# Kernel tuning notes

Measured on AMD Instinct MI355X. Metric: run time of the kernel, lower is better.

Reference implementation:

```python
import jax, jax.numpy as jnp
import numpy as np

T, D_IN, D_OUT, R, S = 8192, 4096, 4096, 16, 16  # tokens, in, out, lora rank, n_stacks
GATE_THRESHOLD = 0.12


def setup_inputs() -> dict:
    key = jax.random.key(0)
    ks = jax.random.split(key, 6)
    x = jax.random.normal(ks[0], (T, D_IN), jnp.float32)
    W = jax.random.normal(ks[1], (D_OUT, D_IN), jnp.float32) * 0.02  # frozen linear weight
    b = jax.random.normal(ks[2], (D_OUT,), jnp.float32) * 0.02       # frozen linear bias
    A = jax.random.normal(ks[3], (S, R, D_IN), jnp.float32) * 0.02   # per-stack lora_A
    B = jax.random.normal(ks[4], (S, D_OUT, R), jnp.float32) * 0.02  # per-stack lora_B
    domain_weights = jax.random.uniform(ks[5], (S,), jnp.float32)    # sigmoid-router weights per domain
    stack_domain = jnp.arange(S, dtype=jnp.int32)                    # stack -> domain index (count=1 each)
    return {"x": x, "W": W, "b": b, "A": A, "B": B,
            "domain_weights": domain_weights, "stack_domain": stack_domain}


def reference(x, W, b, A, B, domain_weights, stack_domain):
    # base frozen linear: out = x @ W^T + b
    base = x @ W.T + b  # [T, D_OUT]
    # threshold-gated per-stack weights: w if w > GATE_THRESHOLD else 0
    g = jnp.where(domain_weights > GATE_THRESHOLD, domain_weights, 0.0)[stack_domain]  # [S]
    # grouped LoRA: stack(x) = (x @ A_s^T) @ B_s^T, combined with gate weights
    h = jnp.einsum('td,srd->str', x, A)          # [S, T, R]
    lora = jnp.einsum('s,str,sor->to', g, h, B)  # [T, D_OUT]
    # original wraps stack contributions in torch.no_grad()
    return base + jax.lax.stop_gradient(lora)
```

## Files before the change

### kernel.cpp

```cpp
#include <hip/hip_runtime.h>
#include <hip/hip_bf16.h>

typedef __bf16 bf16;
typedef __attribute__((ext_vector_type(8))) __bf16 bf16x8;
typedef __attribute__((ext_vector_type(4))) float f32x4;

#define T_TOK 8192
#define DIN   4096
#define DOUT  4096
#define RNK   16
#define NS    16
#define KLORA (NS * RNK)
#define GATE  0.12f

typedef __attribute__((address_space(1))) const void gconst_t;
typedef __attribute__((address_space(3))) void lds_t;

__device__ __forceinline__ void gload_lds16(const void* g, void* l) {
  __builtin_amdgcn_global_load_lds((gconst_t*)g, (lds_t*)l, 16, 0, 0);
}

#define BAR() do { asm volatile("" ::: "memory"); \
                   __builtin_amdgcn_s_barrier();  \
                   asm volatile("" ::: "memory"); } while (0)
#define VMW(n) asm volatile("s_waitcnt vmcnt(" #n ")" ::: "memory")


__global__ __launch_bounds__(256)
void cast_x_kernel(const float* __restrict__ x, bf16* __restrict__ xb) {
  const long i = ((long)blockIdx.x * 256 + threadIdx.x) * 8;
  const float4 v0 = *(const float4*)(x + i);
  const float4 v1 = *(const float4*)(x + i + 4);
  bf16x8 o;
  o[0] = (bf16)v0.x; o[1] = (bf16)v0.y; o[2] = (bf16)v0.z; o[3] = (bf16)v0.w;
  o[4] = (bf16)v1.x; o[5] = (bf16)v1.y; o[6] = (bf16)v1.z; o[7] = (bf16)v1.w;
  *(bf16x8*)(xb + i) = o;
}

__global__ __launch_bounds__(256)
void build_bg_kernel(const float* __restrict__ B, const float* __restrict__ dw,
                     const int* __restrict__ sd, bf16* __restrict__ bg) {
  const int t = blockIdx.x * 256 + threadIdx.x;
  const int o = t >> 8, k = t & 255, s = k >> 4, r = k & 15;
  const float w = dw[sd[s]];
  const float g = (w > GATE) ? w : 0.f;
  bg[t] = (bf16)(g * B[((size_t)s * DOUT + o) * RNK + r]);
}

__global__ __launch_bounds__(256)
void transpose_a_kernel(const float* __restrict__ A, bf16* __restrict__ at) {
  __shared__ float t[32][33];
  const int d0 = blockIdx.x * 32, k0 = blockIdx.y * 32;
  const int tx = threadIdx.x & 31, ty = threadIdx.x >> 5;
#pragma unroll
  for (int i = 0; i < 32; i += 8)
    t[ty + i][tx] = A[(size_t)(k0 + ty + i) * DIN + d0 + tx];
  __syncthreads();
#pragma unroll
  for (int i = 0; i < 32; i += 8)
    at[(size_t)(d0 + ty + i) * KLORA + k0 + tx] = (bf16)t[tx][ty + i];
}

__global__ __launch_bounds__(256)
void gemm_bt(const bf16* __restrict__ Am, const bf16* __restrict__ Bm,
             const float* __restrict__ extra, bf16* __restrict__ outB,
             int M, int N, int K) {
  constexpr int BM = 128, BN = 128, BK = 32;
  __shared__ __align__(16) bf16 At[BM * BK];
  __shared__ __align__(16) bf16 Bt[BN * BK];

  const int tid  = threadIdx.x;
  const int wave = tid >> 6, lane = tid & 63;

  const int nwg = gridDim.x, bid = blockIdx.x;
  const int qq  = nwg >> 3;
  const int sw  = (bid & 7) * qq + (bid >> 3);
  const int ntN = N / BN;
  const long row0 = (long)(sw / ntN) * BM;
  const long col0 = (long)(sw % ntN) * BN;

  f32x4 acc[4][4] = {};
  const int kSteps = K / BK;

  auto stage = [&](int ks) {
    const long k0 = (long)ks * BK;
#pragma unroll
    for (int r = 0; r < 2; ++r) {
      const int off = tid * 16 + r * 4096;
      const int row = off >> 6;
      const int el  = (off & 63) >> 1;
      char* ldsA = (char*)At + (wave << 10) + (r << 12);
      char* ldsB = (char*)Bt + (wave << 10) + (r << 12);
      gload_lds16(Am + (row0 + row) * K + k0 + el, ldsA);
      gload_lds16(Bm + (col0 + row) * K + k0 + el, ldsB);
    }
  };

  stage(0);
  for (int ks = 0; ks < kSteps; ++ks) {
    __syncthreads();
    bf16x8 afr[4], bfr[4];
    const int koff = (lane >> 4) << 3;
    const int rsel = lane & 15;
    const int wr = wave >> 1, wc = wave & 1;
#pragma unroll
    for (int m = 0; m < 4; ++m)
      afr[m] = *(const bf16x8*)&At[((wr << 6) + (m << 4) + rsel) * BK + koff];
#pragma unroll
    for (int n = 0; n < 4; ++n)
      bfr[n] = *(const bf16x8*)&Bt[((wc << 6) + (n << 4) + rsel) * BK + koff];
    __syncthreads();
    if (ks + 1 < kSteps) stage(ks + 1);
#pragma unroll
    for (int m = 0; m < 4; ++m)
#pragma unroll
      for (int n = 0; n < 4; ++n)
        acc[m][n] = __builtin_amdgcn_mfma_f32_16x16x32_bf16(afr[m], bfr[n],
                                                            acc[m][n], 0, 0, 0);
  }

  const int wr = wave >> 1, wc = wave & 1;
#pragma unroll
  for (int m = 0; m < 4; ++m)
#pragma unroll
    for (int n = 0; n < 4; ++n)
#pragma unroll
      for (int j = 0; j < 4; ++j) {
        const long row = row0 + wr * 64 + m * 16 + ((lane >> 4) << 2) + j;
        const long col = col0 + wc * 64 + n * 16 + (lane & 15);
        outB[row * N + col] = (bf16)(acc[m][n][j] + extra[row * N + col]);
      }
}

__global__ __launch_bounds__(512, 2)
void gemm256(const bf16* __restrict__ Am, const bf16* __restrict__ Bm,
             const float* __restrict__ bias, float* __restrict__ out,
             int M, int N, int K) {
  extern __shared__ char smem[];
  const int tid  = threadIdx.x;
  const int wave = tid >> 6, lane = tid & 63;
  const int wr = wave >> 2, wc = wave & 3;
  const int rsel = lane & 15, klane = lane >> 4;

  const int nwg = gridDim.x, bid = blockIdx.x;
  const int sw  = (bid & 7) * (nwg >> 3) + (bid >> 3);
  const int ntN = N >> 8;
  const long row0 = (long)(sw / ntN) << 8;
  const long col0 = (long)(sw % ntN) << 8;

  long srcA[2], srcB[2];
  int  ldsd[2];
  {
    const int rlo = lane >> 2;
    const int kbe = (((lane & 3) * 16) ^ (((lane >> 5) & 1) << 5)) >> 1;
#pragma unroll
    for (int r = 0; r < 2; ++r) {
      const int row = wave * 32 + r * 16 + rlo;
      srcA[r] = (row0 + row) * (long)K + kbe;
      srcB[r] = (col0 + row) * (long)K + kbe;
      ldsd[r] = (wave * 2 + r) << 10;
    }
  }

  const int nT = K >> 6;

  auto stage_half = [&](int H) {
    if (H >= 4 * nT) return;
    const int  slot = H & 7;
    const long kofs = (long)(H >> 2) * 64 + (long)((H >> 1) & 1) * 32;
    if (H & 1) {
#pragma unroll
      for (int r = 0; r < 2; ++r)
        gload_lds16(Bm + srcB[r] + kofs, smem + (slot << 14) + ldsd[r]);
    } else {
#pragma unroll
      for (int r = 0; r < 2; ++r)
        gload_lds16(Am + srcA[r] + kofs, smem + (slot << 14) + ldsd[r]);
    }
  };

  const int laneoff = rsel * 64 + ((klane * 16) ^ ((rsel & 8) << 2));

  f32x4 acc[8][4] = {};
  bf16x8 afr[4], bfr[4];

  auto readA = [&](int slot, int mh) {
    const char* base = smem + (slot << 14) + ((wr * 128 + mh * 64) << 6) + laneoff;
#pragma unroll
    for (int mi = 0; mi < 4; ++mi)
      afr[mi] = *(const bf16x8*)(base + (mi << 10));
  };
  auto readB = [&](int slot) {
    const char* base = smem + (slot << 14) + ((wc * 64) << 6) + laneoff;
#pragma unroll
    for (int n = 0; n < 4; ++n)
      bfr[n] = *(const bf16x8*)(base + (n << 10));
  };
  auto mfma16 = [&](int mh) {
    __builtin_amdgcn_s_setprio(1);
#pragma unroll
    for (int mi = 0; mi < 4; ++mi)
#pragma unroll
      for (int n = 0; n < 4; ++n)
        acc[mh * 4 + mi][n] = __builtin_amdgcn_mfma_f32_16x16x32_bf16(
            afr[mi], bfr[n], acc[mh * 4 + mi][n], 0, 0, 0);
    __builtin_amdgcn_s_setprio(0);
  };

  stage_half(0); stage_half(1); stage_half(2); stage_half(3);
  VMW(4);
  stage_half(4); stage_half(5); stage_half(6);
  VMW(6);
  BAR();

  for (int t = 0; t < nT; ++t) {
    const int b = (t & 1) << 2;
    readB(b | 1); readA(b | 0, 0);
    stage_half(4 * t + 7);
    BAR(); mfma16(0); BAR();
    readA(b | 0, 1);
    stage_half(4 * t + 8);
    BAR(); mfma16(1); BAR();
    readB(b | 3); readA(b | 2, 0);
    stage_half(4 * t + 9);
    BAR(); mfma16(0); BAR();
    readA(b | 2, 1);
    stage_half(4 * t + 10);
    BAR(); mfma16(1);
    if (t == nT - 2) { VMW(0); } else { VMW(6); }
    BAR();
  }

#pragma unroll
  for (int m = 0; m < 8; ++m)
#pragma unroll
    for (int n = 0; n < 4; ++n)
#pragma unroll
      for (int j = 0; j < 4; ++j) {
        const long row = row0 + wr * 128 + m * 16 + klane * 4 + j;
        const long col = col0 + wc * 64 + n * 16 + rsel;
        out[row * N + col] = acc[m][n][j] + bias[col];
      }
}


extern "C" void kernel_launch(void* const* d_in, const int* in_sizes, int n_in,
                              void* d_out, int out_size, void* d_ws, size_t ws_size,
                              hipStream_t stream) {
  (void)in_sizes; (void)n_in; (void)out_size; (void)ws_size;
  const float* x  = (const float*)d_in[0];
  const float* W  = (const float*)d_in[1];
  const float* b  = (const float*)d_in[2];
  const float* A  = (const float*)d_in[3];
  const float* B  = (const float*)d_in[4];
  const float* dw = (const float*)d_in[5];
  const int*   sd = (const int*)d_in[6];
  float* out = (float*)d_out;

  char* ws = (char*)d_ws;
  bf16* xb    = (bf16*)(ws);
  bf16* weff  = (bf16*)(ws + ((size_t)64 << 20));
  bf16* bg    = (bf16*)(ws + ((size_t)96 << 20));
  bf16* acatT = (bf16*)(ws + ((size_t)98 << 20));

  cast_x_kernel<<<(T_TOK * DIN / 8) / 256, 256, 0, stream>>>(x, xb);
  build_bg_kernel<<<(DOUT * KLORA) / 256, 256, 0, stream>>>(B, dw, sd, bg);
  transpose_a_kernel<<<dim3(DIN / 32, KLORA / 32), 256, 0, stream>>>(A, acatT);

  gemm_bt<<<(DOUT / 128) * (DIN / 128), 256, 0, stream>>>(
      bg, acatT, W, weff, DOUT, DIN, KLORA);

  static_assert((T_TOK % 256) == 0 && (DOUT % 256) == 0 && (DIN % 64) == 0, "");
  hipFuncSetAttribute(reinterpret_cast<const void*>(gemm256),
                      hipFuncAttributeMaxDynamicSharedMemorySize, 131072);
  gemm256<<<(T_TOK / 256) * (DOUT / 256), 512, 131072, stream>>>(
      xb, weff, b, out, T_TOK, DOUT, DIN);
}
```

Baseline: 329.5 us.

## Double-buffer LDS fragment registers to overlap reads with MFMA

Splits the A/B register fragments into two sets so the next LDS reads are issued before the current MFMA block runs. Explicit lgkmcnt waits with sched barriers let the MFMAs start while later reads are still outstanding. The vmcnt wait and barriers are moved to match the new order. The cost is more VGPR pressure and a more fragile hand-tuned schedule.

```diff
diff --git a/kernel.cpp b/kernel.cpp
--- a/kernel.cpp
+++ b/kernel.cpp
@@ -24,6 +24,8 @@
                    __builtin_amdgcn_s_barrier();  \
                    asm volatile("" ::: "memory"); } while (0)
 #define VMW(n) asm volatile("s_waitcnt vmcnt(" #n ")" ::: "memory")
+#define LGKM(n) do { asm volatile("s_waitcnt lgkmcnt(" #n ")" ::: "memory"); \
+                     __builtin_amdgcn_sched_barrier(0); } while (0)
 
 
 __global__ __launch_bounds__(256)
@@ -182,52 +184,70 @@
   const int laneoff = rsel * 64 + ((klane * 16) ^ ((rsel & 8) << 2));
 
   f32x4 acc[8][4] = {};
-  bf16x8 afr[4], bfr[4];
-
-  auto readA = [&](int slot, int mh) {
+  bf16x8 afr0[4], afr1[4], bfr0[4], bfr1[4];
+
+  auto readA = [&](int slot, int mh, bf16x8* dst) {
     const char* base = smem + (slot << 14) + ((wr * 128 + mh * 64) << 6) + laneoff;
 #pragma unroll
     for (int mi = 0; mi < 4; ++mi)
-      afr[mi] = *(const bf16x8*)(base + (mi << 10));
-  };
-  auto readB = [&](int slot) {
+      dst[mi] = *(const bf16x8*)(base + (mi << 10));
+  };
+  auto readB = [&](int slot, bf16x8* dst) {
     const char* base = smem + (slot << 14) + ((wc * 64) << 6) + laneoff;
 #pragma unroll
     for (int n = 0; n < 4; ++n)
-      bfr[n] = *(const bf16x8*)(base + (n << 10));
-  };
-  auto mfma16 = [&](int mh) {
+      dst[n] = *(const bf16x8*)(base + (n << 10));
+  };
+  auto mfma16 = [&](int mh, const bf16x8* a, const bf16x8* bf) {
     __builtin_amdgcn_s_setprio(1);
 #pragma unroll
     for (int mi = 0; mi < 4; ++mi)
 #pragma unroll
       for (int n = 0; n < 4; ++n)
         acc[mh * 4 + mi][n] = __builtin_amdgcn_mfma_f32_16x16x32_bf16(
-            afr[mi], bfr[n], acc[mh * 4 + mi][n], 0, 0, 0);
+            a[mi], bf[n], acc[mh * 4 + mi][n], 0, 0, 0);
     __builtin_amdgcn_s_setprio(0);
   };
 
   stage_half(0); stage_half(1); stage_half(2); stage_half(3);
   VMW(4);
+  BAR();
+  readB(1, bfr0); readA(0, 0, afr0);
   stage_half(4); stage_half(5); stage_half(6);
   VMW(6);
   BAR();
 
   for (int t = 0; t < nT; ++t) {
-    const int b = (t & 1) << 2;
-    readB(b | 1); readA(b | 0, 0);
+    const int b  = (t & 1) << 2;
+    const int b2 = b ^ 4;
     stage_half(4 * t + 7);
-    BAR(); mfma16(0); BAR();
-    readA(b | 0, 1);
+    BAR();
+    readA(b | 0, 1, afr1);
+    LGKM(4);
+    mfma16(0, afr0, bfr0);
+    BAR();
     stage_half(4 * t + 8);
-    BAR(); mfma16(1); BAR();
-    readB(b | 3); readA(b | 2, 0);
+    BAR();
+    readB(b | 3, bfr1); readA(b | 2, 0, afr0);
+    LGKM(8);
+    mfma16(1, afr1, bfr0);
+    BAR();
     stage_half(4 * t + 9);
-    BAR(); mfma16(0); BAR();
-    readA(b | 2, 1);
+    BAR();
+    readA(b | 2, 1, afr1);
+    LGKM(4);
+    mfma16(0, afr0, bfr1);
+    if (t == nT - 2) { VMW(0); } else { VMW(4); }
+    BAR();
     stage_half(4 * t + 10);
-    BAR(); mfma16(1);
-    if (t == nT - 2) { VMW(0); } else { VMW(6); }
+    BAR();
+    if (t + 1 < nT) {
+      readB(b2 | 1, bfr0); readA(b2 | 0, 0, afr0);
+      LGKM(8);
+    } else {
+      LGKM(0);
+    }
+    mfma16(1, afr1, bfr1);
     BAR();
   }
 
```

Result: no change. 330.6 us (+0.3%).

## Load B operand directly into registers and interleave LDS reads with MFMAs

Applied to the files above, without the earlier changes.

The GEMM no longer stages the B tile through LDS. Each wave loads its B fragments straight from global memory into double-buffered registers one K-tile ahead, and only A goes through the LDS ring. The main loop is rewritten with sched_barriers so the LDS reads for the next A half-tile are interleaved between MFMA groups, with explicit lgkmcnt waits. This cuts LDS traffic and capacity pressure and overlaps LDS latency with compute, at the cost of more VGPRs, redundant global B loads across the wr waves, and a tightly hand-scheduled pipeline that is fragile to correctness issues.

```diff
diff --git a/kernel.cpp b/kernel.cpp
--- a/kernel.cpp
+++ b/kernel.cpp
@@ -24,6 +24,11 @@
                    __builtin_amdgcn_s_barrier();  \
                    asm volatile("" ::: "memory"); } while (0)
 #define VMW(n) asm volatile("s_waitcnt vmcnt(" #n ")" ::: "memory")
+#define LGKM(n) do { asm volatile("s_waitcnt lgkmcnt(" #n ")" ::: "memory"); \
+                     __builtin_amdgcn_sched_barrier(0); } while (0)
+#define SB0 __builtin_amdgcn_sched_barrier(0)
+#define PRIO1 __builtin_amdgcn_s_setprio(1)
+#define PRIO0 __builtin_amdgcn_s_setprio(0)
 
 
 __global__ __launch_bounds__(256)
@@ -148,7 +153,7 @@
   const long row0 = (long)(sw / ntN) << 8;
   const long col0 = (long)(sw % ntN) << 8;
 
-  long srcA[2], srcB[2];
+  long srcA[2];
   int  ldsd[2];
   {
     const int rlo = lane >> 2;
@@ -157,7 +162,6 @@
     for (int r = 0; r < 2; ++r) {
       const int row = wave * 32 + r * 16 + rlo;
       srcA[r] = (row0 + row) * (long)K + kbe;
-      srcB[r] = (col0 + row) * (long)K + kbe;
       ldsd[r] = (wave * 2 + r) << 10;
     }
   }
@@ -165,71 +169,100 @@
   const int nT = K >> 6;
 
   auto stage_half = [&](int H) {
-    if (H >= 4 * nT) return;
+    if (H >= 2 * nT) return;
     const int  slot = H & 7;
-    const long kofs = (long)(H >> 2) * 64 + (long)((H >> 1) & 1) * 32;
-    if (H & 1) {
-#pragma unroll
-      for (int r = 0; r < 2; ++r)
-        gload_lds16(Bm + srcB[r] + kofs, smem + (slot << 14) + ldsd[r]);
-    } else {
-#pragma unroll
-      for (int r = 0; r < 2; ++r)
-        gload_lds16(Am + srcA[r] + kofs, smem + (slot << 14) + ldsd[r]);
-    }
+    const long kofs = (long)(H >> 1) * 64 + (long)(H & 1) * 32;
+#pragma unroll
+    for (int r = 0; r < 2; ++r)
+      gload_lds16(Am + srcA[r] + kofs, smem + (slot << 14) + ldsd[r]);
   };
 
   const int laneoff = rsel * 64 + ((klane * 16) ^ ((rsel & 8) << 2));
 
   f32x4 acc[8][4] = {};
-  bf16x8 afr[4], bfr[4];
-
-  auto readA = [&](int slot, int mh) {
-    const char* base = smem + (slot << 14) + ((wr * 128 + mh * 64) << 6) + laneoff;
-#pragma unroll
-    for (int mi = 0; mi < 4; ++mi)
-      afr[mi] = *(const bf16x8*)(base + (mi << 10));
-  };
-  auto readB = [&](int slot) {
-    const char* base = smem + (slot << 14) + ((wc * 64) << 6) + laneoff;
-#pragma unroll
-    for (int n = 0; n < 4; ++n)
-      bfr[n] = *(const bf16x8*)(base + (n << 10));
-  };
-  auto mfma16 = [&](int mh) {
-    __builtin_amdgcn_s_setprio(1);
-#pragma unroll
-    for (int mi = 0; mi < 4; ++mi)
-#pragma unroll
-      for (int n = 0; n < 4; ++n)
-        acc[mh * 4 + mi][n] = __builtin_amdgcn_mfma_f32_16x16x32_bf16(
-            afr[mi], bfr[n], acc[mh * 4 + mi][n], 0, 0, 0);
-    __builtin_amdgcn_s_setprio(0);
-  };
-
+  bf16x8 afr0[4], afr1[4];
+  bf16x8 bE[2][4], bO[2][4];
+
+  const bf16* pB0 = Bm + (col0 + wc * 64 + rsel) * (long)K + klane * 8;
+
+#define LOADB8(tt, BUF) do { \
+  const bf16* _p = pB0 + (long)(tt) * 64; \
+  BUF[0][0] = *(const bf16x8*)(_p); \
+  BUF[0][1] = *(const bf16x8*)(_p + 16L * K); \
+  BUF[0][2] = *(const bf16x8*)(_p + 32L * K); \
+  BUF[0][3] = *(const bf16x8*)(_p + 48L * K); \
+  BUF[1][0] = *(const bf16x8*)(_p + 32); \
+  BUF[1][1] = *(const bf16x8*)(_p + 16L * K + 32); \
+  BUF[1][2] = *(const bf16x8*)(_p + 32L * K + 32); \
+  BUF[1][3] = *(const bf16x8*)(_p + 48L * K + 32); \
+} while (0)
+
+#define RDA(slot, mh, mi, dst) \
+  (dst)[(mi)] = *(const bf16x8*)(smem + ((slot) << 14) + \
+                 (((wr << 7) + (mh) * 64 + (mi) * 16) << 6) + laneoff)
+
+#define MB4(mh, mi, A_, Bv) do { \
+  acc[(mh)*4+(mi)][0] = __builtin_amdgcn_mfma_f32_16x16x32_bf16((A_)[(mi)], (Bv)[0], acc[(mh)*4+(mi)][0], 0, 0, 0); \
+  acc[(mh)*4+(mi)][1] = __builtin_amdgcn_mfma_f32_16x16x32_bf16((A_)[(mi)], (Bv)[1], acc[(mh)*4+(mi)][1], 0, 0, 0); \
+  acc[(mh)*4+(mi)][2] = __builtin_amdgcn_mfma_f32_16x16x32_bf16((A_)[(mi)], (Bv)[2], acc[(mh)*4+(mi)][2], 0, 0, 0); \
+  acc[(mh)*4+(mi)][3] = __builtin_amdgcn_mfma_f32_16x16x32_bf16((A_)[(mi)], (Bv)[3], acc[(mh)*4+(mi)][3], 0, 0, 0); \
+} while (0)
+
+#define TILE_BODY(t, BUSE, BLOAD) do { \
+  const int _s0 = (2 * (t)) & 7, _s1 = _s0 | 1, _s2 = (2 * (t) + 2) & 7; \
+  const bool _last = ((t) == nT - 1); \
+   \
+  BAR(); LGKM(0); PRIO1; \
+  MB4(0, 0, afr0, (BUSE)[0]); SB0; RDA(_s0, 1, 0, afr1); SB0; \
+  MB4(0, 1, afr0, (BUSE)[0]); SB0; RDA(_s0, 1, 1, afr1); SB0; \
+  MB4(0, 2, afr0, (BUSE)[0]); SB0; RDA(_s0, 1, 2, afr1); SB0; \
+  MB4(0, 3, afr0, (BUSE)[0]); SB0; RDA(_s0, 1, 3, afr1); PRIO0; \
+   \
+  BAR(); stage_half(2 * (t) + 4); SB0; \
+  if (!_last) { LOADB8((t) + 1, BLOAD); } SB0; \
+  LGKM(0); PRIO1; \
+  MB4(1, 0, afr1, (BUSE)[0]); SB0; RDA(_s1, 0, 0, afr0); SB0; \
+  MB4(1, 1, afr1, (BUSE)[0]); SB0; RDA(_s1, 0, 1, afr0); SB0; \
+  MB4(1, 2, afr1, (BUSE)[0]); SB0; RDA(_s1, 0, 2, afr0); SB0; \
+  MB4(1, 3, afr1, (BUSE)[0]); SB0; RDA(_s1, 0, 3, afr0); PRIO0; \
+   \
+  BAR(); LGKM(0); PRIO1; \
+  MB4(0, 0, afr0, (BUSE)[1]); SB0; RDA(_s1, 1, 0, afr1); SB0; \
+  MB4(0, 1, afr0, (BUSE)[1]); SB0; RDA(_s1, 1, 1, afr1); SB0; \
+  MB4(0, 2, afr0, (BUSE)[1]); SB0; RDA(_s1, 1, 2, afr1); SB0; \
+  MB4(0, 3, afr0, (BUSE)[1]); SB0; RDA(_s1, 1, 3, afr1); PRIO0; \
+   \
+  BAR(); stage_half(2 * (t) + 5); SB0; \
+  LGKM(0); PRIO1; \
+  if (!_last) { \
+    MB4(1, 0, afr1, (BUSE)[1]); SB0; RDA(_s2, 0, 0, afr0); SB0; \
+    MB4(1, 1, afr1, (BUSE)[1]); SB0; RDA(_s2, 0, 1, afr0); SB0; \
+    MB4(1, 2, afr1, (BUSE)[1]); SB0; RDA(_s2, 0, 2, afr0); SB0; \
+    MB4(1, 3, afr1, (BUSE)[1]); SB0; RDA(_s2, 0, 3, afr0); \
+  } else { \
+    MB4(1, 0, afr1, (BUSE)[1]); MB4(1, 1, afr1, (BUSE)[1]); \
+    MB4(1, 2, afr1, (BUSE)[1]); MB4(1, 3, afr1, (BUSE)[1]); \
+  } \
+  PRIO0; \
+  VMW(2); \
+} while (0)
+
+  LOADB8(0, bE);
+  SB0;
   stage_half(0); stage_half(1); stage_half(2); stage_half(3);
-  VMW(4);
-  stage_half(4); stage_half(5); stage_half(6);
-  VMW(6);
+  VMW(2);
   BAR();
-
-  for (int t = 0; t < nT; ++t) {
-    const int b = (t & 1) << 2;
-    readB(b | 1); readA(b | 0, 0);
-    stage_half(4 * t + 7);
-    BAR(); mfma16(0); BAR();
-    readA(b | 0, 1);
-    stage_half(4 * t + 8);
-    BAR(); mfma16(1); BAR();
-    readB(b | 3); readA(b | 2, 0);
-    stage_half(4 * t + 9);
-    BAR(); mfma16(0); BAR();
-    readA(b | 2, 1);
-    stage_half(4 * t + 10);
-    BAR(); mfma16(1);
-    if (t == nT - 2) { VMW(0); } else { VMW(6); }
-    BAR();
+  RDA(0, 0, 0, afr0); RDA(0, 0, 1, afr0); RDA(0, 0, 2, afr0); RDA(0, 0, 3, afr0);
+
+  for (int u = 0; u < nT; u += 2) {
+    TILE_BODY(u,     bE, bO);
+    TILE_BODY(u + 1, bO, bE);
   }
+
+#undef TILE_BODY
+#undef MB4
+#undef RDA
+#undef LOADB8
 
 #pragma unroll
   for (int m = 0; m < 8; ++m)
```

After: 1.311 ms. 298% more time.
